# Kernel tuning notes

Measured on AMD Instinct MI355X. Metric: run time of the kernel, lower is better.

## Reference

```python
import jax, jax.numpy as jnp
import numpy as np

N_NODES = 100_000
N_EDGES = 1_600_000
N_GRAPHS = 64
EPS = 1e-7  # GENConv message epsilon
D_IN, D_H, D_OUT, OUT_DIM = 128, 192, 128, 10


def _w(k, fan_in, fan_out):
    return jax.random.normal(k, (fan_in, fan_out), jnp.float32) * (1.0 / np.sqrt(fan_in))


def setup_inputs() -> dict:
    key = jax.random.key(0)
    ks = jax.random.split(key, 8)
    return {
        "x": jax.random.normal(ks[0], (N_NODES, D_IN), jnp.float32),
        "W0": _w(ks[1], D_IN, D_H), "b0": jnp.zeros((D_H,), jnp.float32),
        "W1": _w(ks[2], D_H, D_H), "b1": jnp.zeros((D_H,), jnp.float32),
        "W2": _w(ks[3], D_H, D_H), "b2": jnp.zeros((D_H,), jnp.float32),
        "W3": _w(ks[4], D_H, D_OUT), "b3": jnp.zeros((D_OUT,), jnp.float32),
        "Wfc": _w(ks[5], D_OUT, OUT_DIM), "bfc": jnp.zeros((OUT_DIM,), jnp.float32),
        "edge_index": jax.random.randint(ks[6], (2, N_EDGES), 0, N_NODES, jnp.int32),
        "batch": jnp.sort(jax.random.randint(ks[7], (N_NODES,), 0, N_GRAPHS, jnp.int32)),
    }


def _genconv(x, W, b, src, dst):
    # GENConv (num_layers=1, aggr='add'): message = relu(x_j) + eps,
    # scatter-add to dst, residual add, single Linear MLP.
    msg = jax.nn.relu(x[src]) + EPS          # [E, d]
    agg = jax.ops.segment_sum(msg, dst, num_segments=N_NODES)  # [N, d]
    return (x + agg) @ W + b


def reference(x, W0, b0, W1, b1, W2, b2, W3, b3, Wfc, bfc, edge_index, batch):
    src, dst = edge_index[0], edge_index[1]  # source_to_target flow
    for W, b in ((W0, b0), (W1, b1), (W2, b2), (W3, b3)):
        x = _genconv(x, W, b, src, dst)
    # global mean pool over graphs
    sums = jax.ops.segment_sum(x, batch, num_segments=N_GRAPHS)
    counts = jax.ops.segment_sum(jnp.ones((x.shape[0],), x.dtype), batch,
                                 num_segments=N_GRAPHS)
    pooled = sums / jnp.maximum(counts, 1.0)[:, None]  # [G, D_OUT]
    logits = pooled @ Wfc + bfc                        # [G, OUT_DIM]
    return jax.nn.log_softmax(logits, axis=1)
```

## Files before the change

kernel.cpp:

```cpp
#include <hip/hip_runtime.h>
#include <hip/hip_bf16.h>
#include <stdint.h>

constexpr int NN = 100000;
constexpr int NE = 1600000;
constexpr int NG = 64;
constexpr int S  = 192;
constexpr int NB_SCAN = 98;
constexpr unsigned int ZOFF = (unsigned int)NN * 384u;

constexpr int PREP_CONVX_BLK = 12500;
constexpr int PREP_INDEG_BLK = 1563;
constexpr int PREP_CONVW_BLK = 384;
constexpr int PREP_GB_BLK    = 391;
constexpr int PREP_GRID = PREP_CONVX_BLK + PREP_INDEG_BLK + PREP_CONVW_BLK + PREP_GB_BLK;

constexpr int EG_BLOCKS = 391;
constexpr int HROW = 50048;

typedef __bf16 bf16x8 __attribute__((ext_vector_type(8)));
typedef float  f32x16 __attribute__((ext_vector_type(16)));
typedef float  f32x2  __attribute__((ext_vector_type(2)));

union U16x4 { uint4 u; bf16x8 b; };

__device__ __forceinline__ float bl(unsigned int u) { return __uint_as_float(u << 16); }
__device__ __forceinline__ float bh(unsigned int u) { return __uint_as_float(u & 0xffff0000u); }
__device__ __forceinline__ float b16f(unsigned short u) { return __uint_as_float(((unsigned int)u) << 16); }
__device__ __forceinline__ unsigned int fb(float f) {
    unsigned int u = __float_as_uint(f);
    return (u + 0x7fffu + ((u >> 16) & 1u)) >> 16;
}
__device__ __forceinline__ unsigned int prelu(unsigned int u) {
    unsigned int r;
    asm("v_pk_max_f16 %0, %1, %2" : "=v"(r) : "v"(u), "v"(0u));
    return r;
}
__device__ __forceinline__ unsigned int cnt2bf(unsigned int h) {
    float f0 = (float)(h & 0xffffu);
    float f1 = (float)(h >> 16);
    return (__float_as_uint(f0) >> 16) | (__float_as_uint(f1) & 0xffff0000u);
}

__global__ __launch_bounds__(256) void k_prep(const float* __restrict__ x,
                                              const int* __restrict__ ei,
                                              const int* __restrict__ bat,
                                              const float* __restrict__ W0, const float* __restrict__ W1,
                                              const float* __restrict__ W2,
                                              unsigned short* __restrict__ A_,
                                              int* __restrict__ indeg, int* __restrict__ slot,
                                              unsigned short* __restrict__ T0, unsigned short* __restrict__ T1,
                                              unsigned short* __restrict__ T2,
                                              int* __restrict__ nstart) {
    const int b = blockIdx.x;
    if (b < PREP_CONVX_BLK) {
        int id = b * 256 + threadIdx.x;
        if (id < 96) ((unsigned int*)(A_ + (size_t)NN * S))[id] = 0u;
        int row = id >> 5, c4 = id & 31;
        float4 v = ((const float4*)x)[id];
        uint2 a;
        a.x = fb(v.x) | (fb(v.y) << 16);
        a.y = fb(v.z) | (fb(v.w) << 16);
        *(uint2*)(A_ + row * S + c4 * 4) = a;
    } else if (b < PREP_CONVX_BLK + PREP_INDEG_BLK) {
        int e4 = ((b - PREP_CONVX_BLK) * 256 + threadIdx.x) * 4;
        if (e4 < NE) {
            int4 d = *(const int4*)(ei + NE + e4);
            int4 sl;
            sl.x = atomicAdd(&indeg[d.x], 1);
            sl.y = atomicAdd(&indeg[d.y], 1);
            sl.z = atomicAdd(&indeg[d.z], 1);
            sl.w = atomicAdd(&indeg[d.w], 1);
            *(int4*)(slot + e4) = sl;
        }
    } else if (b < PREP_CONVX_BLK + PREP_INDEG_BLK + PREP_CONVW_BLK) {
        int id = (b - PREP_CONVX_BLK - PREP_INDEG_BLK) * 256 + threadIdx.x;
        const float* W; unsigned short* T; int N, base;
        if      (id < 24576) { W = W0; T = T0; N = 192; base = 0;     }
        else if (id < 61440) { W = W1; T = T1; N = 192; base = 24576; }
        else                 { W = W2; T = T2; N = 192; base = 61440; }
        int lid = id - base;
        int ci = lid >> 3, j = lid & 7;
        int kc = ci / N, n = ci % N;
        T[lid] = (unsigned short)fb(W[(kc * 8 + j) * N + n]);
    } else {
        int n = (b - PREP_CONVX_BLK - PREP_INDEG_BLK - PREP_CONVW_BLK) * 256 + threadIdx.x;
        if (n < NN) {
            int b0 = bat[n];
            int bprev = (n == 0) ? -1 : bat[n - 1];
            for (int g = bprev + 1; g <= b0; g++) nstart[g] = n;
            if (n == NN - 1)
                for (int g = b0 + 1; g < NG; g++) nstart[g] = NN;
        }
    }
}

__global__ __launch_bounds__(1024) void k_scan1(const int* __restrict__ indeg, int* __restrict__ offs,
                                                int* __restrict__ partials) {
    __shared__ int s[1024];
    int t = threadIdx.x;
    int gid = blockIdx.x * 1024 + t;
    int v = (gid < NN) ? indeg[gid] : 0;
    s[t] = v;
    __syncthreads();
    for (int d = 1; d < 1024; d <<= 1) {
        int tv = (t >= d) ? s[t - d] : 0;
        __syncthreads();
        s[t] += tv;
        __syncthreads();
    }
    if (gid < NN) offs[gid + 1] = s[t];
    if (t == 1023) partials[blockIdx.x] = s[1023];
}

__global__ __launch_bounds__(128) void k_scan2(int* __restrict__ offs, int* __restrict__ partials) {
    __shared__ int s[128];
    int t = threadIdx.x;
    int v = (t < NB_SCAN) ? partials[t] : 0;
    s[t] = v;
    __syncthreads();
    for (int d = 1; d < 128; d <<= 1) {
        int tv = (t >= d) ? s[t - d] : 0;
        __syncthreads();
        s[t] += tv;
        __syncthreads();
    }
    if (t < NB_SCAN) partials[t] = s[t] - v;
    if (t == 0) offs[0] = 0;
}

__global__ __launch_bounds__(1024) void k_scan3(int* __restrict__ offs, const int* __restrict__ partials) {
    int gid = blockIdx.x * 1024 + threadIdx.x;
    if (gid < NN) offs[gid + 1] += partials[blockIdx.x];
}

__global__ __launch_bounds__(256) void k_fill(const int* __restrict__ ei, const int* __restrict__ offs,
                                              const int* __restrict__ slot, int* __restrict__ csr) {
    int e4 = (blockIdx.x * 256 + threadIdx.x) * 4;
    if (e4 >= NE) return;
    int4 sv = *(const int4*)(ei + e4);
    int4 dv = *(const int4*)(ei + NE + e4);
    int4 sl = *(const int4*)(slot + e4);
    csr[offs[dv.x] + sl.x] = sv.x;
    csr[offs[dv.y] + sl.y] = sv.y;
    csr[offs[dv.z] + sl.z] = sv.z;
    csr[offs[dv.w] + sl.w] = sv.w;
}

__global__ __launch_bounds__(256, 8) void k_agg192(const unsigned short* __restrict__ Ain,
                                                   unsigned short* __restrict__ Yout,
                                                   const int* __restrict__ offs,
                                                   const int* __restrict__ indeg,
                                                   const int* __restrict__ csr) {
    const int w = threadIdx.x >> 6, lane = threadIdx.x & 63;
    const int i = __builtin_amdgcn_readfirstlane(blockIdx.x * 4 + w);
    const bool act = lane < 48;
    const int deg   = __builtin_amdgcn_readfirstlane(indeg[i]);
    const int start = __builtin_amdgcn_readfirstlane(offs[i]);
    const int fo = (act ? lane : 47) * 8;
    const char* Ab = (const char*)Ain;

    f32x2 A01, A23;
    {
        uint2 p = *(const uint2*)(Ab + (size_t)i * 384 + fo);
        const float ed = 1e-7f * (float)deg;
        A01 = (f32x2){bl(p.x) + ed, bh(p.x) + ed};
        A23 = (f32x2){bl(p.y) + ed, bh(p.y) + ed};
    }

    const int* ecsr = csr + start;
    for (int e = 0; e < deg; e += 16) {
        unsigned int off[16];
#pragma unroll
        for (int k = 0; k < 16; k++) {
            int v = ecsr[e + k];
            off[k] = (e + k < deg) ? (unsigned int)v * 384u : ZOFF;
        }
        uint2 p[16];
#pragma unroll
        for (int k = 0; k < 16; k++)
            p[k] = *(const uint2*)(Ab + (size_t)off[k] + fo);
#pragma unroll
        for (int k = 0; k < 16; k++) {
            unsigned int rx = prelu(p[k].x), ry = prelu(p[k].y);
            A01 += (f32x2){bl(rx), bh(rx)};
            A23 += (f32x2){bl(ry), bh(ry)};
        }
    }
    if (act) {
        uint2 o;
        o.x = fb(A01.x) | (fb(A01.y) << 16);
        o.y = fb(A23.x) | (fb(A23.y) << 16);
        *(uint2*)(Yout + (size_t)i * S + lane * 4) = o;
    }
}

__global__ __launch_bounds__(256, 8) void k_agg128(const unsigned short* __restrict__ Ain,
                                                   unsigned short* __restrict__ Yout,
                                                   const int* __restrict__ offs,
                                                   const int* __restrict__ indeg,
                                                   const int* __restrict__ csr) {
    const int w = threadIdx.x >> 6, lane = threadIdx.x & 63;
    const int i = __builtin_amdgcn_readfirstlane(blockIdx.x * 4 + w);
    const int deg   = __builtin_amdgcn_readfirstlane(indeg[i]);
    const int start = __builtin_amdgcn_readfirstlane(offs[i]);
    const int fo = lane * 4;
    const char* Ab = (const char*)Ain;

    f32x2 A01;
    {
        unsigned int p = *(const unsigned int*)(Ab + (size_t)i * 384 + fo);
        const float ed = 1e-7f * (float)deg;
        A01 = (f32x2){bl(p) + ed, bh(p) + ed};
    }

    const int* ecsr = csr + start;
    for (int e = 0; e < deg; e += 16) {
        unsigned int off[16];
#pragma unroll
        for (int k = 0; k < 16; k++) {
            int v = ecsr[e + k];
            off[k] = (e + k < deg) ? (unsigned int)v * 384u : ZOFF;
        }
        unsigned int q[16];
#pragma unroll
        for (int k = 0; k < 16; k++)
            q[k] = *(const unsigned int*)(Ab + (size_t)off[k] + fo);
#pragma unroll
        for (int k = 0; k < 16; k++) {
            unsigned int r = prelu(q[k]);
            A01 += (f32x2){bl(r), bh(r)};
        }
    }
    *(unsigned int*)(Yout + (size_t)i * S + lane * 2) =
        fb(A01.x) | (fb(A01.y) << 16);
}

template <int K, int N>
__global__ __launch_bounds__(256) void k_gemm(const unsigned short* __restrict__ Yin,
                                              const unsigned short* __restrict__ WtC,
                                              const float* __restrict__ bias,
                                              unsigned short* __restrict__ Aout) {
    static_assert(K % 16 == 0 && N % 32 == 0, "");
    const int w = threadIdx.x >> 6, lane = threadIdx.x & 63;
    const int rt = blockIdx.x * 4 + w;
    if (rt >= (NN / 32)) return;
    const int hl = lane >> 5, lr = lane & 31;
    const int row0 = rt * 32;
    f32x16 acc[N / 32];
#pragma unroll
    for (int c = 0; c < N / 32; c++)
#pragma unroll
        for (int r = 0; r < 16; r++) acc[c][r] = 0.f;

    const unsigned short* ap = Yin + (row0 + lr) * S + hl * 8;
    const uint4* b4 = (const uint4*)WtC;
#pragma unroll
    for (int ks = 0; ks < K / 16; ks++) {
        U16x4 a;
        a.u = *(const uint4*)(ap + ks * 16);
#pragma unroll
        for (int c = 0; c < N / 32; c++) {
            U16x4 b;
            b.u = b4[(ks * 2 + hl) * N + c * 32 + lr];
            acc[c] = __builtin_amdgcn_mfma_f32_32x32x16_bf16(a.b, b.b, acc[c], 0, 0, 0);
        }
    }
#pragma unroll
    for (int c = 0; c < N / 32; c++) {
        const int col = c * 32 + lr;
        const float bc = bias[col];
#pragma unroll
        for (int r = 0; r < 16; r++) {
            const int row = row0 + (r & 3) + 8 * (r >> 2) + 4 * hl;
            Aout[row * S + col] = (unsigned short)fb(acc[c][r] + bc);
        }
    }
}

__global__ __launch_bounds__(256) void k_hist(const int* __restrict__ csr, const int* __restrict__ offs,
                                              const int* __restrict__ nstart,
                                              unsigned int* __restrict__ hist) {
    const int g = blockIdx.x >> 2, q = blockIdx.x & 3;
    const int s0 = offs[nstart[g]];
    const int s1 = (g == NG - 1) ? NE : offs[nstart[g + 1]];
    const int len = s1 - s0;
    const int qs = s0 + (int)(((long long)len * q) >> 2);
    const int qe = s0 + (int)(((long long)len * (q + 1)) >> 2);
    unsigned int* hrow = hist + (size_t)g * HROW;
    for (int p = qs + threadIdx.x; p < qe; p += 256) {
        int src = csr[p];
        atomicAdd(&hrow[src >> 1], 1u << (16 * (src & 1)));
    }
}

__global__ __launch_bounds__(384) void k_egemm(const unsigned short* __restrict__ A0,
                                               const unsigned int* __restrict__ hist,
                                               float* __restrict__ partials) {
    const int wv = threadIdx.x >> 6, lane = threadIdx.x & 63;
    const int b = blockIdx.x;
    const int j0 = b * 256;
    const int hl = lane >> 5, lr = lane & 31;
    const int feat = wv * 32 + lr;
    f32x16 acc[2];
#pragma unroll
    for (int m = 0; m < 2; m++)
#pragma unroll
        for (int r = 0; r < 16; r++) acc[m][r] = 0.f;

    for (int kk = 0; kk < 16; kk++) {
        const int jh = (j0 >> 1) + kk * 8 + hl * 4;
        U16x4 af[2];
#pragma unroll
        for (int m = 0; m < 2; m++) {
            uint4 h = *(const uint4*)(hist + (size_t)(m * 32 + lr) * HROW + jh);
            af[m].u = (uint4){cnt2bf(h.x), cnt2bf(h.y), cnt2bf(h.z), cnt2bf(h.w)};
        }
        U16x4 bf;
#pragma unroll
        for (int tp = 0; tp < 4; tp++) {
            int je = j0 + kk * 16 + hl * 8 + tp * 2;
            int ja = min(je, NN), jb = min(je + 1, NN);
            unsigned int u0 = A0[(size_t)ja * S + feat];
            unsigned int u1 = A0[(size_t)jb * S + feat];
            ((unsigned int*)&bf.u)[tp] = prelu(u0 | (u1 << 16));
        }
#pragma unroll
        for (int m = 0; m < 2; m++)
            acc[m] = __builtin_amdgcn_mfma_f32_32x32x16_bf16(af[m].b, bf.b, acc[m], 0, 0, 0);
    }
    float* pb = partials + (size_t)b * 12288;
#pragma unroll
    for (int m = 0; m < 2; m++)
#pragma unroll
        for (int r = 0; r < 16; r++) {
            const int g = m * 32 + (r & 3) + 8 * (r >> 2) + 4 * hl;
            pb[g * 192 + feat] = acc[m][r];
        }
}

__global__ __launch_bounds__(256) void k_reduce(const float* __restrict__ partials,
                                                float* __restrict__ msg) {
    int gf = blockIdx.x * 256 + threadIdx.x;
    if (gf >= 12288) return;
    float s = 0.f;
    for (int p = 0; p < EG_BLOCKS; p++)
        s += partials[(size_t)p * 12288 + gf];
    msg[gf] = s;
}

__global__ __launch_bounds__(192) void k_pool(const unsigned short* __restrict__ A_,
                                              const int* __restrict__ batch,
                                              const int* __restrict__ indeg,
                                              float* __restrict__ sums, float* __restrict__ cnt,
                                              float* __restrict__ degsum) {
    const int b = blockIdx.x;
    const int f = threadIdx.x;
    int n0 = b * 200;
    int n1 = min(n0 + 200, NN);
    int cur = batch[n0];
    float acc = 0.f;
    int run = 0, dacc = 0;
    for (int n = n0; n < n1; n++) {
        int g = batch[n];
        if (g != cur) {
            atomicAdd(&sums[cur * 192 + f], acc);
            if (f == 0) { atomicAdd(&cnt[cur], (float)run); atomicAdd(&degsum[cur], (float)dacc); }
            acc = 0.f; run = 0; dacc = 0; cur = g;
        }
        acc += b16f(A_[(size_t)n * S + f]);
        run++;
        if (f == 0) dacc += indeg[n];
    }
    atomicAdd(&sums[cur * 192 + f], acc);
    if (f == 0) { atomicAdd(&cnt[cur], (float)run); atomicAdd(&degsum[cur], (float)dacc); }
}

__global__ __launch_bounds__(128) void k_head(const float* __restrict__ sums, const float* __restrict__ msg,
                                              const float* __restrict__ cnt, const float* __restrict__ degsum,
                                              const float* __restrict__ W3, const float* __restrict__ b3,
                                              const float* __restrict__ Wfc, const float* __restrict__ bfc,
                                              float* __restrict__ out) {
    __shared__ float py[192];
    __shared__ float tl[128];
    __shared__ float lg[10];
    const int g = blockIdx.x, t = threadIdx.x;
    const float inv = 1.f / fmaxf(cnt[g], 1.f);
    const float ed = 1e-7f * degsum[g];
    for (int k = t; k < 192; k += 128)
        py[k] = (sums[g * 192 + k] + msg[g * 192 + k] + ed) * inv;
    __syncthreads();
    float tf = b3[t];
    for (int k = 0; k < 192; k++) tf += py[k] * W3[k * 128 + t];
    tl[t] = tf;
    __syncthreads();
    if (t < 10) {
        float s = bfc[t];
        for (int f = 0; f < 128; f++) s += tl[f] * Wfc[f * 10 + t];
        lg[t] = s;
    }
    __syncthreads();
    if (t < 10) {
        float m = lg[0];
        for (int k = 1; k < 10; k++) m = fmaxf(m, lg[k]);
        float se = 0.f;
        for (int k = 0; k < 10; k++) se += expf(lg[k] - m);
        out[g * 10 + t] = lg[t] - m - logf(se);
    }
}

constexpr size_t A0_OFF     = 0;
constexpr size_t A1_OFF     = 38400384;
constexpr size_t HIST_REL   = 0;
constexpr size_t PARTS_REL  = 12812288;
constexpr size_t CSR_OFF    = 76800384;
constexpr size_t OFFS_OFF   = 83200384;
constexpr size_t INDEG_OFF  = 83600512;
constexpr size_t PART_OFF   = 84000512;
constexpr size_t NSTART_OFF = 84001024;
constexpr size_t WT0_OFF    = 84001280;
constexpr size_t WT1_OFF    = 84050432;
constexpr size_t WT2_OFF    = 84124160;
constexpr size_t SUMS_OFF   = 84197888;
constexpr size_t CNT_OFF    = 84247040;
constexpr size_t DEGS_OFF   = 84247296;
constexpr size_t MSG_OFF    = 84247552;

extern "C" void kernel_launch(void* const* d_in, const int* in_sizes, int n_in,
                              void* d_out, int out_size, void* d_ws, size_t ws_size,
                              hipStream_t stream) {
    const float* x   = (const float*)d_in[0];
    const float* W0  = (const float*)d_in[1];
    const float* b0  = (const float*)d_in[2];
    const float* W1  = (const float*)d_in[3];
    const float* b1  = (const float*)d_in[4];
    const float* W2  = (const float*)d_in[5];
    const float* b2  = (const float*)d_in[6];
    const float* W3  = (const float*)d_in[7];
    const float* b3  = (const float*)d_in[8];
    const float* Wfc = (const float*)d_in[9];
    const float* bfc = (const float*)d_in[10];
    const int*   ei  = (const int*)d_in[11];
    const int*   bat = (const int*)d_in[12];
    float* out = (float*)d_out;

    char* ws = (char*)d_ws;
    unsigned short* A0  = (unsigned short*)(ws + A0_OFF);
    unsigned short* A1  = (unsigned short*)(ws + A1_OFF);
    int* slot   = (int*)(ws + A1_OFF);
    unsigned int* hist  = (unsigned int*)(ws + A1_OFF + HIST_REL);
    float* parts        = (float*)(ws + A1_OFF + PARTS_REL);
    int* csr    = (int*)(ws + CSR_OFF);
    int* offs   = (int*)(ws + OFFS_OFF);
    int* indeg  = (int*)(ws + INDEG_OFF);
    int* part   = (int*)(ws + PART_OFF);
    int* nstart = (int*)(ws + NSTART_OFF);
    unsigned short* Wt0 = (unsigned short*)(ws + WT0_OFF);
    unsigned short* Wt1 = (unsigned short*)(ws + WT1_OFF);
    unsigned short* Wt2 = (unsigned short*)(ws + WT2_OFF);
    float* sums   = (float*)(ws + SUMS_OFF);
    float* cnt    = (float*)(ws + CNT_OFF);
    float* degsum = (float*)(ws + DEGS_OFF);
    float* msg    = (float*)(ws + MSG_OFF);

    hipMemsetAsync(ws + INDEG_OFF, 0, 400000, stream);
    hipMemsetAsync(ws + SUMS_OFF, 0, 49664, stream);

    k_prep<<<PREP_GRID, 256, 0, stream>>>(x, ei, bat, W0, W1, W2, A0, indeg, slot,
                                          Wt0, Wt1, Wt2, nstart);

    k_scan1<<<NB_SCAN, 1024, 0, stream>>>(indeg, offs, part);
    k_scan2<<<1, 128, 0, stream>>>(offs, part);
    k_scan3<<<NB_SCAN, 1024, 0, stream>>>(offs, part);
    k_fill<<<(NE / 4 + 255) / 256, 256, 0, stream>>>(ei, offs, slot, csr);

    const int AGG_GRID  = NN / 4;
    const int GEMM_GRID = (NN / 32 + 3) / 4;

    k_agg128<<<AGG_GRID, 256, 0, stream>>>(A0, A1, offs, indeg, csr);
    k_gemm<128, 192><<<GEMM_GRID, 256, 0, stream>>>(A1, Wt0, b0, A0);
    k_agg192<<<AGG_GRID, 256, 0, stream>>>(A0, A1, offs, indeg, csr);
    k_gemm<192, 192><<<GEMM_GRID, 256, 0, stream>>>(A1, Wt1, b1, A0);
    k_agg192<<<AGG_GRID, 256, 0, stream>>>(A0, A1, offs, indeg, csr);
    k_gemm<192, 192><<<GEMM_GRID, 256, 0, stream>>>(A1, Wt2, b2, A0);

    hipMemsetAsync(ws + A1_OFF + HIST_REL, 0, 12812288, stream);
    k_hist<<<NG * 4, 256, 0, stream>>>(csr, offs, nstart, hist);
    k_egemm<<<EG_BLOCKS, 384, 0, stream>>>(A0, hist, parts);
    k_reduce<<<48, 256, 0, stream>>>(parts, msg);
    k_pool<<<500, 192, 0, stream>>>(A0, bat, indeg, sums, cnt, degsum);
    k_head<<<NG, 128, 0, stream>>>(sums, msg, cnt, degsum, W3, b3, Wfc, bfc, out);
}
```

Before: 712.8 us.

## Store activations in 16-feature column chunks and aggregate per chunk

```diff
diff --git a/kernel.cpp b/kernel.cpp
--- a/kernel.cpp
+++ b/kernel.cpp
@@ -5,9 +5,12 @@
 constexpr int NN = 100000;
 constexpr int NE = 1600000;
 constexpr int NG = 64;
-constexpr int S  = 192;
 constexpr int NB_SCAN = 98;
-constexpr unsigned int ZOFF = (unsigned int)NN * 384u;
+
+constexpr int ST0 = NN + 1;
+constexpr int ST1 = NN;
+constexpr size_t CB0 = (size_t)ST0 * 32;
+constexpr size_t CB1 = (size_t)ST1 * 32;
 
 constexpr int PREP_CONVX_BLK = 12500;
 constexpr int PREP_INDEG_BLK = 1563;
@@ -20,7 +23,8 @@
 
 typedef __bf16 bf16x8 __attribute__((ext_vector_type(8)));
 typedef float  f32x16 __attribute__((ext_vector_type(16)));
-typedef float  f32x2  __attribute__((ext_vector_type(2)));
+typedef float  f32x4  __attribute__((ext_vector_type(4)));
+typedef unsigned int u32x2 __attribute__((ext_vector_type(2)));
 
 union U16x4 { uint4 u; bf16x8 b; };
 
@@ -55,13 +59,18 @@
     const int b = blockIdx.x;
     if (b < PREP_CONVX_BLK) {
         int id = b * 256 + threadIdx.x;
-        if (id < 96) ((unsigned int*)(A_ + (size_t)NN * S))[id] = 0u;
-        int row = id >> 5, c4 = id & 31;
-        float4 v = ((const float4*)x)[id];
+        if (id < 96) {
+            int cc = id >> 3, u = id & 7;
+            ((unsigned int*)(A_ + ((size_t)cc * ST0 + NN) * 16))[u] = 0u;
+        }
+        int cc = id / 400000;
+        int r  = id - cc * 400000;
+        int node = r >> 2, q = r & 3;
+        float4 v = ((const float4*)x)[node * 32 + cc * 4 + q];
         uint2 a;
         a.x = fb(v.x) | (fb(v.y) << 16);
         a.y = fb(v.z) | (fb(v.w) << 16);
-        *(uint2*)(A_ + row * S + c4 * 4) = a;
+        *(uint2*)(A_ + ((size_t)cc * ST0 + node) * 16 + q * 4) = a;
     } else if (b < PREP_CONVX_BLK + PREP_INDEG_BLK) {
         int e4 = ((b - PREP_CONVX_BLK) * 256 + threadIdx.x) * 4;
         if (e4 < NE) {
@@ -147,93 +156,73 @@
     csr[offs[dv.w] + sl.w] = sv.w;
 }
 
-__global__ __launch_bounds__(256, 8) void k_agg192(const unsigned short* __restrict__ Ain,
-                                                   unsigned short* __restrict__ Yout,
-                                                   const int* __restrict__ offs,
-                                                   const int* __restrict__ indeg,
-                                                   const int* __restrict__ csr) {
-    const int w = threadIdx.x >> 6, lane = threadIdx.x & 63;
-    const int i = __builtin_amdgcn_readfirstlane(blockIdx.x * 4 + w);
-    const bool act = lane < 48;
-    const int deg   = __builtin_amdgcn_readfirstlane(indeg[i]);
-    const int start = __builtin_amdgcn_readfirstlane(offs[i]);
-    const int fo = (act ? lane : 47) * 8;
-    const char* Ab = (const char*)Ain;
-
-    f32x2 A01, A23;
+template <int CH>
+__global__ __launch_bounds__(256, 8) void k_aggc(const unsigned short* __restrict__ Ain,
+                                                 unsigned short* __restrict__ Yout,
+                                                 const int* __restrict__ offs,
+                                                 const int* __restrict__ indeg,
+                                                 const int* __restrict__ csr) {
+    constexpr int IPX = CH / 4;
+    constexpr int NBH = 782;
+    const int x   = blockIdx.x & 7;
+    const int jj  = blockIdx.x >> 3;
+    const int il  = jj / NBH;
+    const int nbl = jj - il * NBH;
+    const int item = x * IPX + il;
+    const int c = item >> 1, h = item & 1;
+    const int l = threadIdx.x & 63, wv = threadIdx.x >> 6;
+    const int g = l >> 2, q = l & 3;
+    const int node = h * 50048 + nbl * 64 + wv * 16 + g;
+    const bool valid = node < NN;
+    const unsigned nd = valid ? (unsigned)node : (unsigned)NN;
+    const int deg   = valid ? indeg[node] : 0;
+    const int start = valid ? offs[node] : 0;
+    const char* Ab = (const char*)Ain + (size_t)c * CB0;
+    const unsigned qo = (unsigned)(q * 8);
+
+    f32x4 acc;
     {
-        uint2 p = *(const uint2*)(Ab + (size_t)i * 384 + fo);
+        uint2 p = *(const uint2*)(Ab + nd * 32u + qo);
         const float ed = 1e-7f * (float)deg;
-        A01 = (f32x2){bl(p.x) + ed, bh(p.x) + ed};
-        A23 = (f32x2){bl(p.y) + ed, bh(p.y) + ed};
-    }
-
-    const int* ecsr = csr + start;
-    for (int e = 0; e < deg; e += 16) {
-        unsigned int off[16];
-#pragma unroll
-        for (int k = 0; k < 16; k++) {
-            int v = ecsr[e + k];
-            off[k] = (e + k < deg) ? (unsigned int)v * 384u : ZOFF;
-        }
-        uint2 p[16];
-#pragma unroll
-        for (int k = 0; k < 16; k++)
-            p[k] = *(const uint2*)(Ab + (size_t)off[k] + fo);
-#pragma unroll
-        for (int k = 0; k < 16; k++) {
-            unsigned int rx = prelu(p[k].x), ry = prelu(p[k].y);
-            A01 += (f32x2){bl(rx), bh(rx)};
-            A23 += (f32x2){bl(ry), bh(ry)};
-        }
-    }
-    if (act) {
-        uint2 o;
-        o.x = fb(A01.x) | (fb(A01.y) << 16);
-        o.y = fb(A23.x) | (fb(A23.y) << 16);
-        *(uint2*)(Yout + (size_t)i * S + lane * 4) = o;
-    }
-}
-
-__global__ __launch_bounds__(256, 8) void k_agg128(const unsigned short* __restrict__ Ain,
-                                                   unsigned short* __restrict__ Yout,
-                                                   const int* __restrict__ offs,
-                                                   const int* __restrict__ indeg,
-                                                   const int* __restrict__ csr) {
-    const int w = threadIdx.x >> 6, lane = threadIdx.x & 63;
-    const int i = __builtin_amdgcn_readfirstlane(blockIdx.x * 4 + w);
-    const int deg   = __builtin_amdgcn_readfirstlane(indeg[i]);
-    const int start = __builtin_amdgcn_readfirstlane(offs[i]);
-    const int fo = lane * 4;
-    const char* Ab = (const char*)Ain;
-
-    f32x2 A01;
-    {
-        unsigned int p = *(const unsigned int*)(Ab + (size_t)i * 384 + fo);
-        const float ed = 1e-7f * (float)deg;
-        A01 = (f32x2){bl(p) + ed, bh(p) + ed};
-    }
-
-    const int* ecsr = csr + start;
-    for (int e = 0; e < deg; e += 16) {
-        unsigned int off[16];
-#pragma unroll
-        for (int k = 0; k < 16; k++) {
-            int v = ecsr[e + k];
-            off[k] = (e + k < deg) ? (unsigned int)v * 384u : ZOFF;
-        }
-        unsigned int q[16];
-#pragma unroll
-        for (int k = 0; k < 16; k++)
-            q[k] = *(const unsigned int*)(Ab + (size_t)off[k] + fo);
-#pragma unroll
-        for (int k = 0; k < 16; k++) {
-            unsigned int r = prelu(q[k]);
-            A01 += (f32x2){bl(r), bh(r)};
-        }
-    }
-    *(unsigned int*)(Yout + (size_t)i * S + lane * 2) =
-        fb(A01.x) | (fb(A01.y) << 16);
+        acc = (f32x4){bl(p.x) + ed, bh(p.x) + ed, bl(p.y) + ed, bh(p.y) + ed};
+    }
+
+    const int* ec = csr + start;
+    int v0 = __builtin_nontemporal_load(ec + 0);
+    int v1 = __builtin_nontemporal_load(ec + 1);
+    int v2 = __builtin_nontemporal_load(ec + 2);
+    int v3 = __builtin_nontemporal_load(ec + 3);
+    for (int e = 0; __any(e < deg); e += 4) {
+        const int w0 = __builtin_nontemporal_load(ec + e + 4);
+        const int w1 = __builtin_nontemporal_load(ec + e + 5);
+        const int w2 = __builtin_nontemporal_load(ec + e + 6);
+        const int w3 = __builtin_nontemporal_load(ec + e + 7);
+        const unsigned n0 = (e + 0 < deg) ? (unsigned)v0 : (unsigned)NN;
+        const unsigned n1 = (e + 1 < deg) ? (unsigned)v1 : (unsigned)NN;
+        const unsigned n2 = (e + 2 < deg) ? (unsigned)v2 : (unsigned)NN;
+        const unsigned n3 = (e + 3 < deg) ? (unsigned)v3 : (unsigned)NN;
+        uint2 p0 = *(const uint2*)(Ab + n0 * 32u + qo);
+        uint2 p1 = *(const uint2*)(Ab + n1 * 32u + qo);
+        uint2 p2 = *(const uint2*)(Ab + n2 * 32u + qo);
+        uint2 p3 = *(const uint2*)(Ab + n3 * 32u + qo);
+        unsigned r;
+        r = prelu(p0.x); acc.x += bl(r); acc.y += bh(r);
+        r = prelu(p0.y); acc.z += bl(r); acc.w += bh(r);
+        r = prelu(p1.x); acc.x += bl(r); acc.y += bh(r);
+        r = prelu(p1.y); acc.z += bl(r); acc.w += bh(r);
+        r = prelu(p2.x); acc.x += bl(r); acc.y += bh(r);
+        r = prelu(p2.y); acc.z += bl(r); acc.w += bh(r);
+        r = prelu(p3.x); acc.x += bl(r); acc.y += bh(r);
+        r = prelu(p3.y); acc.z += bl(r); acc.w += bh(r);
+        v0 = w0; v1 = w1; v2 = w2; v3 = w3;
+    }
+    if (valid) {
+        u32x2 o;
+        o.x = fb(acc.x) | (fb(acc.y) << 16);
+        o.y = fb(acc.z) | (fb(acc.w) << 16);
+        __builtin_nontemporal_store(o,
+            (u32x2*)((char*)Yout + (size_t)c * CB1 + (unsigned)node * 32u + qo));
+    }
 }
 
 template <int K, int N>
@@ -253,12 +242,12 @@
 #pragma unroll
         for (int r = 0; r < 16; r++) acc[c][r] = 0.f;
 
-    const unsigned short* ap = Yin + (row0 + lr) * S + hl * 8;
+    const unsigned short* ap = Yin + (size_t)(row0 + lr) * 16 + hl * 8;
     const uint4* b4 = (const uint4*)WtC;
 #pragma unroll
     for (int ks = 0; ks < K / 16; ks++) {
         U16x4 a;
-        a.u = *(const uint4*)(ap + ks * 16);
+        a.u = *(const uint4*)(ap + (size_t)ks * (ST1 * 16));
 #pragma unroll
         for (int c = 0; c < N / 32; c++) {
             U16x4 b;
@@ -270,10 +259,11 @@
     for (int c = 0; c < N / 32; c++) {
         const int col = c * 32 + lr;
         const float bc = bias[col];
+        const int cc = col >> 4, co = col & 15;
 #pragma unroll
         for (int r = 0; r < 16; r++) {
             const int row = row0 + (r & 3) + 8 * (r >> 2) + 4 * hl;
-            Aout[row * S + col] = (unsigned short)fb(acc[c][r] + bc);
+            Aout[((size_t)cc * ST0 + row) * 16 + co] = (unsigned short)fb(acc[c][r] + bc);
         }
     }
 }
@@ -302,6 +292,7 @@
     const int j0 = b * 256;
     const int hl = lane >> 5, lr = lane & 31;
     const int feat = wv * 32 + lr;
+    const size_t fof = (size_t)(feat >> 4) * (ST0 * 16) + (feat & 15);
     f32x16 acc[2];
 #pragma unroll
     for (int m = 0; m < 2; m++)
@@ -316,18 +307,18 @@
             uint4 h = *(const uint4*)(hist + (size_t)(m * 32 + lr) * HROW + jh);
             af[m].u = (uint4){cnt2bf(h.x), cnt2bf(h.y), cnt2bf(h.z), cnt2bf(h.w)};
         }
-        U16x4 bf;
+        U16x4 bf_;
 #pragma unroll
         for (int tp = 0; tp < 4; tp++) {
             int je = j0 + kk * 16 + hl * 8 + tp * 2;
             int ja = min(je, NN), jb = min(je + 1, NN);
-            unsigned int u0 = A0[(size_t)ja * S + feat];
-            unsigned int u1 = A0[(size_t)jb * S + feat];
-            ((unsigned int*)&bf.u)[tp] = prelu(u0 | (u1 << 16));
+            unsigned int u0 = A0[fof + (size_t)ja * 16];
+            unsigned int u1 = A0[fof + (size_t)jb * 16];
+            ((unsigned int*)&bf_.u)[tp] = prelu(u0 | (u1 << 16));
         }
 #pragma unroll
         for (int m = 0; m < 2; m++)
-            acc[m] = __builtin_amdgcn_mfma_f32_32x32x16_bf16(af[m].b, bf.b, acc[m], 0, 0, 0);
+            acc[m] = __builtin_amdgcn_mfma_f32_32x32x16_bf16(af[m].b, bf_.b, acc[m], 0, 0, 0);
     }
     float* pb = partials + (size_t)b * 12288;
 #pragma unroll
@@ -356,6 +347,7 @@
                                               float* __restrict__ degsum) {
     const int b = blockIdx.x;
     const int f = threadIdx.x;
+    const unsigned short* Af = A_ + (size_t)(f >> 4) * (ST0 * 16) + (f & 15);
     int n0 = b * 200;
     int n1 = min(n0 + 200, NN);
     int cur = batch[n0];
@@ -368,7 +360,7 @@
             if (f == 0) { atomicAdd(&cnt[cur], (float)run); atomicAdd(&degsum[cur], (float)dacc); }
             acc = 0.f; run = 0; dacc = 0; cur = g;
         }
-        acc += b16f(A_[(size_t)n * S + f]);
+        acc += b16f(Af[(size_t)n * 16]);
         run++;
         if (f == 0) dacc += indeg[n];
     }
@@ -474,14 +466,15 @@
     k_scan3<<<NB_SCAN, 1024, 0, stream>>>(offs, part);
     k_fill<<<(NE / 4 + 255) / 256, 256, 0, stream>>>(ei, offs, slot, csr);
 
-    const int AGG_GRID  = NN / 4;
     const int GEMM_GRID = (NN / 32 + 3) / 4;
-
-    k_agg128<<<AGG_GRID, 256, 0, stream>>>(A0, A1, offs, indeg, csr);
+    constexpr int AGG8_GRID  = 8 * 2 * 782;
+    constexpr int AGG12_GRID = 8 * 3 * 782;
+
+    k_aggc<8><<<AGG8_GRID, 256, 0, stream>>>(A0, A1, offs, indeg, csr);
     k_gemm<128, 192><<<GEMM_GRID, 256, 0, stream>>>(A1, Wt0, b0, A0);
-    k_agg192<<<AGG_GRID, 256, 0, stream>>>(A0, A1, offs, indeg, csr);
+    k_aggc<12><<<AGG12_GRID, 256, 0, stream>>>(A0, A1, offs, indeg, csr);
     k_gemm<192, 192><<<GEMM_GRID, 256, 0, stream>>>(A1, Wt1, b1, A0);
-    k_agg192<<<AGG_GRID, 256, 0, stream>>>(A0, A1, offs, indeg, csr);
+    k_aggc<12><<<AGG12_GRID, 256, 0, stream>>>(A0, A1, offs, indeg, csr);
     k_gemm<192, 192><<<GEMM_GRID, 256, 0, stream>>>(A1, Wt2, b2, A0);
 
     hipMemsetAsync(ws + A1_OFF + HIST_REL, 0, 12812288, stream);
```

New measurement: 991.0 us. 1.39x slower.
